# Kernel optimization log

Hardware: AMD Instinct MI355X
Metric: run time of the kernel (lower is better)

## Reference

```python
import jax, jax.numpy as jnp
import numpy as np

B, T, E, A = 16, 512, 256, 8

def setup_inputs() -> dict:
    key = jax.random.key(0)
    k1, k2, k3, k4, k5 = jax.random.split(key, 5)
    sent_feat = jax.random.normal(k1, (B, T, E), dtype=jnp.float32)
    mask = jax.random.randint(k2, (B, T), 0, 2, dtype=jnp.int32)
    atr_scores = jax.random.uniform(k3, (B, A), dtype=jnp.float32)
    W = jax.random.normal(k4, (E, A * E), dtype=jnp.float32) * 0.02  # nn.Linear weight (out, in)
    b = jax.random.normal(k5, (E,), dtype=jnp.float32) * 0.02
    return {"sent_feat": sent_feat, "mask": mask, "atr_scores": atr_scores, "W": W, "b": b}

def reference(sent_feat, mask, atr_scores, W, b):
    Bb, Tt, Ee = sent_feat.shape
    Aa = atr_scores.shape[1]
    sqrt_dim = jnp.float32(np.sqrt(Ee))
    # scale per-attribute copies of the sentence features: (B,A,T,E)
    sf = sent_feat[:, None, :, :] * atr_scores[:, :, None, None]
    sf = sf.reshape(Bb * Aa, Tt, Ee)
    # scaled dot-product scores (B*A, T, T)
    score = jnp.einsum('bte,bse->bts', sf, sf) / sqrt_dim
    # outer-product mask: bmm(mask[:,:,1], mask[:,1,:]) -> bool, repeat over A
    mf = mask.astype(jnp.float32)
    m2 = (mf[:, :, None] * mf[:, None, :]) != 0.0  # (B,T,T)
    m2 = jnp.broadcast_to(m2[:, None, :, :], (Bb, Aa, Tt, Tt)).reshape(Bb * Aa, Tt, Tt)
    # masked_fill_ fills score with 0.0 where mask == 0 (NOT -inf, faithful to source)
    score = jnp.where(m2, score, jnp.float32(0.0))
    # softmax(score - global_max) over last axis
    attn = jax.nn.softmax(score - jnp.max(score), axis=-1)
    attn_out = jnp.einsum('bts,bse->bte', attn, sf)  # (B*A, T, E)
    attn_out = attn_out.reshape(Bb, Tt, Aa * Ee)
    output = attn_out @ W.T + b  # (B, T, E)
    return (output, attn)
```

## Files before the change

kernel.cpp:

```cpp
#include <hip/hip_runtime.h>
#include <hip/hip_bf16.h>


#define Bt 16
#define Tt 512
#define Et 256
#define At 8

typedef __attribute__((ext_vector_type(8))) short short8;
typedef __attribute__((ext_vector_type(4))) float floatx4;

static __device__ __forceinline__ unsigned short f2bf(float x) {
    union { float f; unsigned u; } v; v.f = x;
    unsigned r = v.u + 0x7fffu + ((v.u >> 16) & 1u);
    return (unsigned short)(r >> 16);
}

static __device__ __forceinline__ floatx4 mfma16(short8 a, short8 b, floatx4 c) {
    return __builtin_amdgcn_mfma_f32_16x16x32_bf16(a, b, c, 0, 0, 0);
}

static __device__ __forceinline__ void barrier_lds() {
    __builtin_amdgcn_sched_barrier(0);
    asm volatile("s_waitcnt lgkmcnt(0)" ::: "memory");
    __builtin_amdgcn_s_barrier();
    __builtin_amdgcn_sched_barrier(0);
}

__global__ __launch_bounds__(256) void k_prep_sent(const float* __restrict__ sent,
                                                   unsigned short* __restrict__ sentG,
                                                   unsigned short* __restrict__ sentFB) {
    int bb = blockIdx.z;
    int s0 = blockIdx.x * 32;
    int e0 = blockIdx.y * 32;
    __shared__ float tile[32][33];
    int c  = threadIdx.x & 31;
    int r4 = threadIdx.x >> 5;
    for (int i = 0; i < 4; ++i) {
        int r = r4 + 8 * i;
        tile[r][c] = sent[(bb * Tt + s0 + r) * Et + e0 + c];
    }
    __syncthreads();
    int wv = threadIdx.x >> 6, lane = threadIdx.x & 63, quad = lane >> 4, l16 = lane & 15;
    union { short8 s; unsigned short e[8]; } u;
    if (wv < 2) {
#pragma unroll
        for (int j = 0; j < 8; ++j) u.e[j] = f2bf(tile[wv * 16 + l16][quad * 8 + j]);
        *(short8*)(sentG + (((size_t)(bb * 32 + (s0 >> 4) + wv)) * 8 + (e0 >> 5)) * 512
                   + lane * 8) = u.s;
    } else {
        int h = wv - 2;
#pragma unroll
        for (int j = 0; j < 8; ++j) u.e[j] = f2bf(tile[quad * 8 + j][h * 16 + l16]);
        *(short8*)(sentFB + (((size_t)(bb * 16 + (e0 >> 4) + h)) * 16 + (s0 >> 5)) * 512
                   + lane * 8) = u.s;
    }
}

__global__ __launch_bounds__(256) void k_prep_w(const float* __restrict__ W,
                                                unsigned short* __restrict__ Wp) {
    int nt = blockIdx.x;
    int pc = blockIdx.y;
    int wave = threadIdx.x >> 6, lane = threadIdx.x & 63, quad = lane >> 4, l16 = lane & 15;
    const int KK = At * Et;
    for (int p = pc * 2; p < pc * 2 + 2; ++p) {
        int kc = wave + 4 * p;
        const float* src = W + (size_t)(nt * 16 + l16) * KK + kc * 32 + quad * 8;
        union { short8 s; unsigned short e[8]; } u;
#pragma unroll
        for (int j = 0; j < 8; ++j) u.e[j] = f2bf(src[j]);
        *(short8*)(Wp + (((size_t)nt * 64 + kc) << 9) + lane * 8) = u.s;
    }
}

__global__ __launch_bounds__(256) void k_attnpv(const unsigned short* __restrict__ sentG,
                                                const unsigned short* __restrict__ sentFB,
                                                const int* __restrict__ mask,
                                                const float* __restrict__ atr,
                                                float* __restrict__ attnf,
                                                unsigned short* __restrict__ XwsF) {
    int hw = blockIdx.x;
    int logical = (hw & 7) * 128 + (hw >> 3);
    int bb = logical >> 6;
    int z  = (logical >> 5) & 1;
    int t0 = (logical & 31) * 16;
    int a0 = z * 4;
    __shared__ float S[16][516];
    __shared__ float msk[512];
    __shared__ float mrowv[16];
    unsigned short* Pb  = (unsigned short*)&S[0][0];
    unsigned short* Xb2 = Pb + 8192;

    int tid = threadIdx.x;
    for (int i = tid; i < 512; i += 256) msk[i] = (mask[bb * Tt + i] != 0) ? 1.0f : 0.0f;
    if (tid < 16) mrowv[tid] = (mask[bb * Tt + t0 + tid] != 0) ? 1.0f : 0.0f;
    barrier_lds();

    int wv = tid >> 6, lane = tid & 63, quad = lane >> 4, l16 = lane & 15;

    const unsigned short* Gbase = sentG + ((size_t)(bb * 32 + (t0 >> 4)) * 8) * 512 + lane * 8;
    short8 af[8];
#pragma unroll
    for (int kk = 0; kk < 8; ++kk) af[kk] = *(const short8*)(Gbase + kk * 512);

#pragma unroll
    for (int i = 0; i < 8; ++i) {
        int nt = wv * 8 + i;
        const unsigned short* Bb = sentG + ((size_t)(bb * 32 + nt) * 8) * 512 + lane * 8;
        floatx4 c = {0.f, 0.f, 0.f, 0.f};
#pragma unroll
        for (int kk = 0; kk < 8; ++kk)
            c = mfma16(af[kk], *(const short8*)(Bb + kk * 512), c);
#pragma unroll
        for (int r = 0; r < 4; ++r) {
            int cidx = nt * 16 + l16;
            S[quad * 4 + r][cidx] = c[r] * msk[cidx] * mrowv[quad * 4 + r];
        }
    }
    barrier_lds();

    int row = tid >> 4, cl = tid & 15;
    float w[32];
    float wmax = -1e30f;
#pragma unroll
    for (int i4 = 0; i4 < 8; ++i4) {
        float4 v = *(const float4*)&S[row][i4 * 64 + cl * 4];
        w[i4 * 4 + 0] = v.x; w[i4 * 4 + 1] = v.y; w[i4 * 4 + 2] = v.z; w[i4 * 4 + 3] = v.w;
        wmax = fmaxf(wmax, fmaxf(fmaxf(v.x, v.y), fmaxf(v.z, v.w)));
    }
#pragma unroll
    for (int off = 8; off >= 1; off >>= 1) wmax = fmaxf(wmax, __shfl_xor(wmax, off, 64));
    barrier_lds();

    int L = (t0 >> 3) & 15;

    for (int a = a0; a < a0 + 4; ++a) {
        float av = atr[bb * At + a];
        float coef = av * av * (1.0f / 16.0f);
        float mx = coef * wmax;
        float p[32];
        float sum = 0.f;
#pragma unroll
        for (int j = 0; j < 32; ++j) {
            float e = __expf(fmaf(coef, w[j], -mx));
            p[j] = e;
            sum += e;
        }
#pragma unroll
        for (int off = 8; off >= 1; off >>= 1) sum += __shfl_xor(sum, off, 64);
        float inv = 1.0f / sum;
#pragma unroll
        for (int j = 0; j < 32; ++j) p[j] *= inv;

        float* orow = attnf + ((size_t)(bb * At + a) * Tt + (t0 + row)) * Tt;
#pragma unroll
        for (int i4 = 0; i4 < 8; ++i4) {
            float4 v;
            v.x = p[i4 * 4 + 0]; v.y = p[i4 * 4 + 1];
            v.z = p[i4 * 4 + 2]; v.w = p[i4 * 4 + 3];
            *(float4*)(orow + i4 * 64 + cl * 4) = v;
        }

#pragma unroll
        for (int i4 = 0; i4 < 8; ++i4) {
            unsigned b0 = __float_as_uint(p[i4 * 4 + 0]) + 0x8000u;
            unsigned b1 = __float_as_uint(p[i4 * 4 + 1]) + 0x8000u;
            unsigned b2 = __float_as_uint(p[i4 * 4 + 2]) + 0x8000u;
            unsigned b3 = __float_as_uint(p[i4 * 4 + 3]) + 0x8000u;
            uint2 pk;
            pk.x = __builtin_amdgcn_perm(b1, b0, 0x07060302u);
            pk.y = __builtin_amdgcn_perm(b3, b2, 0x07060302u);
            int h = i4 * 8 + (cl >> 1);
            *(uint2*)(Pb + row * 512 + ((h ^ (row & 7)) << 3) + (cl & 1) * 4) = pk;
        }
        barrier_lds();

        floatx4 pacc[4];
#pragma unroll
        for (int i = 0; i < 4; ++i) pacc[i] = (floatx4){0.f, 0.f, 0.f, 0.f};
        for (int kc = 0; kc < 16; ++kc) {
            short8 afr = *(const short8*)(Pb + l16 * 512 +
                (((kc * 4 + quad) ^ (l16 & 7)) << 3));
#pragma unroll
            for (int i = 0; i < 4; ++i) {
                short8 bfr = *(const short8*)(sentFB +
                    (((size_t)(bb * 16 + wv * 4 + i) * 16 + kc) << 9) + lane * 8);
                pacc[i] = mfma16(afr, bfr, pacc[i]);
            }
        }

#pragma unroll
        for (int i = 0; i < 4; ++i) {
            int W16 = wv * 4 + i;
            int kcb = W16 >> 1;
            int qp  = (W16 & 1) * 2 + (l16 >> 3);
            int jp  = l16 & 7;
#pragma unroll
            for (int r = 0; r < 4; ++r) {
                int tl = quad * 4 + r;
                Xb2[(((tl & 7) * 8 + kcb) << 6) + qp * 16 + ((tl >> 3) << 3) + jp]
                    = f2bf(av * pacc[i][r]);
            }
        }
        barrier_lds();

        {
            int kc = tid >> 2, qp = tid & 3;
            int TPT = (a << 2) + (t0 >> 7);
            size_t base = (((size_t)(bb * 32 + TPT)) * 64 + kc) * 512;
            short8 v0 = *(const short8*)(Xb2 + (kc << 6) + qp * 16);
            short8 v1 = *(const short8*)(Xb2 + (kc << 6) + qp * 16 + 8);
            *(short8*)(XwsF + base + (qp * 16 + L) * 8)     = v0;
            *(short8*)(XwsF + base + (qp * 16 + L + 1) * 8) = v1;
        }
    }
}

__global__ __launch_bounds__(256) void k_out(const unsigned short* __restrict__ XwsF,
                                             const unsigned short* __restrict__ Wp,
                                             const float* __restrict__ bias,
                                             float* __restrict__ out) {
    int hw = blockIdx.x;
    int logical = (hw & 7) * 128 + (hw >> 3);
    int bb  = logical >> 6;
    int TPT = (logical >> 1) & 31;
    int nh  = logical & 1;
    int tid = threadIdx.x;
    int wv = tid >> 6, lane = tid & 63, quad = lane >> 4, l16 = lane & 15;

    const unsigned short* Abase = XwsF + ((size_t)(bb * 32 + TPT)) * 64 * 512 + lane * 8;
    floatx4 oacc[2];
    oacc[0] = (floatx4){0.f, 0.f, 0.f, 0.f};
    oacc[1] = (floatx4){0.f, 0.f, 0.f, 0.f};
    int nt0 = nh * 8 + wv * 2;
#pragma unroll 4
    for (int kc = 0; kc < 64; ++kc) {
        short8 afr = *(const short8*)(Abase + kc * 512);
#pragma unroll
        for (int i = 0; i < 2; ++i) {
            short8 bf = *(const short8*)(Wp +
                (((size_t)(nt0 + i) * 64 + kc) << 9) + lane * 8);
            oacc[i] = mfma16(afr, bf, oacc[i]);
        }
    }
#pragma unroll
    for (int i = 0; i < 2; ++i) {
        int n = (nt0 + i) * 16 + l16;
        float bv = bias[n];
#pragma unroll
        for (int r = 0; r < 4; ++r) {
            int tp = TPT * 16 + quad * 4 + r;
            out[((size_t)bb * Tt + tp) * Et + n] = oacc[i][r] + bv;
        }
    }
}

extern "C" void kernel_launch(void* const* d_in, const int* in_sizes, int n_in,
                              void* d_out, int out_size, void* d_ws, size_t ws_size,
                              hipStream_t stream) {
    const float* sent = (const float*)d_in[0];
    const int*   mask = (const int*)d_in[1];
    const float* atr  = (const float*)d_in[2];
    const float* W    = (const float*)d_in[3];
    const float* bias = (const float*)d_in[4];

    float* out0  = (float*)d_out;
    float* attnf = out0 + (size_t)Bt * Tt * Et;

    char* ws = (char*)d_ws;
    unsigned short* sentG  = (unsigned short*)(ws);
    unsigned short* sentFB = (unsigned short*)(ws + 4194304);
    unsigned short* Wp     = (unsigned short*)(ws + 8388608);
    unsigned short* XwsF   = (unsigned short*)(ws + 9437184);

    hipLaunchKernelGGL(k_prep_sent, dim3(Tt / 32, Et / 32, Bt), dim3(256), 0, stream,
                       sent, sentG, sentFB);
    hipLaunchKernelGGL(k_prep_w, dim3(16, 8), dim3(256), 0, stream, W, Wp);
    hipLaunchKernelGGL(k_attnpv, dim3(1024), dim3(256), 0, stream,
                       sentG, sentFB, mask, atr, attnf, XwsF);
    hipLaunchKernelGGL(k_out, dim3(1024), dim3(256), 0, stream,
                       XwsF, Wp, bias, out0);
}
```

Measured before the change: 232.6 us.

## Batch four attribute P tiles in LDS and share B-fragment loads across them

The attention-PV kernel now writes softmax probabilities for all four attributes into separate LDS tiles before a single barrier. It then runs one PV MFMA loop that loads each sentFB fragment once and reuses it across the four attributes, with a 4x4 accumulator array. Epilogue packing and global stores are also batched per attribute, which removes several barriers per attribute iteration. The cost is a larger LDS footprint (64 KB buffer) and 64 accumulator registers, which may reduce occupancy or cause spills.

```diff
diff --git a/kernel.cpp b/kernel.cpp
--- a/kernel.cpp
+++ b/kernel.cpp
@@ -85,11 +85,12 @@
     int z  = (logical >> 5) & 1;
     int t0 = (logical & 31) * 16;
     int a0 = z * 4;
-    __shared__ float S[16][516];
+
+    __shared__ __align__(16) float Sbuf[16384];
     __shared__ float msk[512];
     __shared__ float mrowv[16];
-    unsigned short* Pb  = (unsigned short*)&S[0][0];
-    unsigned short* Xb2 = Pb + 8192;
+    unsigned short* Pb  = (unsigned short*)Sbuf;
+    unsigned short* Xb2 = (unsigned short*)Sbuf;
 
     int tid = threadIdx.x;
     for (int i = tid; i < 512; i += 256) msk[i] = (mask[bb * Tt + i] != 0) ? 1.0f : 0.0f;
@@ -114,7 +115,7 @@
 #pragma unroll
         for (int r = 0; r < 4; ++r) {
             int cidx = nt * 16 + l16;
-            S[quad * 4 + r][cidx] = c[r] * msk[cidx] * mrowv[quad * 4 + r];
+            Sbuf[(quad * 4 + r) * 516 + cidx] = c[r] * msk[cidx] * mrowv[quad * 4 + r];
         }
     }
     barrier_lds();
@@ -124,7 +125,7 @@
     float wmax = -1e30f;
 #pragma unroll
     for (int i4 = 0; i4 < 8; ++i4) {
-        float4 v = *(const float4*)&S[row][i4 * 64 + cl * 4];
+        float4 v = *(const float4*)&Sbuf[row * 516 + i4 * 64 + cl * 4];
         w[i4 * 4 + 0] = v.x; w[i4 * 4 + 1] = v.y; w[i4 * 4 + 2] = v.z; w[i4 * 4 + 3] = v.w;
         wmax = fmaxf(wmax, fmaxf(fmaxf(v.x, v.y), fmaxf(v.z, v.w)));
     }
@@ -134,7 +135,9 @@
 
     int L = (t0 >> 3) & 15;
 
-    for (int a = a0; a < a0 + 4; ++a) {
+#pragma unroll
+    for (int al = 0; al < 4; ++al) {
+        int a = a0 + al;
         float av = atr[bb * At + a];
         float coef = av * av * (1.0f / 16.0f);
         float mx = coef * wmax;
@@ -171,24 +174,38 @@
             pk.x = __builtin_amdgcn_perm(b1, b0, 0x07060302u);
             pk.y = __builtin_amdgcn_perm(b3, b2, 0x07060302u);
             int h = i4 * 8 + (cl >> 1);
-            *(uint2*)(Pb + row * 512 + ((h ^ (row & 7)) << 3) + (cl & 1) * 4) = pk;
-        }
-        barrier_lds();
-
-        floatx4 pacc[4];
-#pragma unroll
-        for (int i = 0; i < 4; ++i) pacc[i] = (floatx4){0.f, 0.f, 0.f, 0.f};
-        for (int kc = 0; kc < 16; ++kc) {
-            short8 afr = *(const short8*)(Pb + l16 * 512 +
+            *(uint2*)(Pb + al * 8192 + row * 512 + ((h ^ (row & 7)) << 3)
+                      + (cl & 1) * 4) = pk;
+        }
+    }
+    barrier_lds();
+
+    floatx4 acc[4][4];
+#pragma unroll
+    for (int al = 0; al < 4; ++al)
+#pragma unroll
+        for (int i = 0; i < 4; ++i) acc[al][i] = (floatx4){0.f, 0.f, 0.f, 0.f};
+
+    for (int kc = 0; kc < 16; ++kc) {
+        short8 bfr[4];
+#pragma unroll
+        for (int i = 0; i < 4; ++i)
+            bfr[i] = *(const short8*)(sentFB +
+                (((size_t)(bb * 16 + wv * 4 + i) * 16 + kc) << 9) + lane * 8);
+#pragma unroll
+        for (int al = 0; al < 4; ++al) {
+            short8 afr = *(const short8*)(Pb + al * 8192 + l16 * 512 +
                 (((kc * 4 + quad) ^ (l16 & 7)) << 3));
 #pragma unroll
-            for (int i = 0; i < 4; ++i) {
-                short8 bfr = *(const short8*)(sentFB +
-                    (((size_t)(bb * 16 + wv * 4 + i) * 16 + kc) << 9) + lane * 8);
-                pacc[i] = mfma16(afr, bfr, pacc[i]);
-            }
-        }
-
+            for (int i = 0; i < 4; ++i)
+                acc[al][i] = mfma16(afr, bfr[i], acc[al][i]);
+        }
+    }
+    barrier_lds();
+
+#pragma unroll
+    for (int al = 0; al < 4; ++al) {
+        float av = atr[bb * At + a0 + al];
 #pragma unroll
         for (int i = 0; i < 4; ++i) {
             int W16 = wv * 4 + i;
@@ -198,21 +215,23 @@
 #pragma unroll
             for (int r = 0; r < 4; ++r) {
                 int tl = quad * 4 + r;
-                Xb2[(((tl & 7) * 8 + kcb) << 6) + qp * 16 + ((tl >> 3) << 3) + jp]
-                    = f2bf(av * pacc[i][r]);
+                Xb2[al * 4096 + (((tl & 7) * 8 + kcb) << 6) + qp * 16
+                    + ((tl >> 3) << 3) + jp] = f2bf(av * acc[al][i][r]);
             }
         }
-        barrier_lds();
-
-        {
-            int kc = tid >> 2, qp = tid & 3;
-            int TPT = (a << 2) + (t0 >> 7);
-            size_t base = (((size_t)(bb * 32 + TPT)) * 64 + kc) * 512;
-            short8 v0 = *(const short8*)(Xb2 + (kc << 6) + qp * 16);
-            short8 v1 = *(const short8*)(Xb2 + (kc << 6) + qp * 16 + 8);
-            *(short8*)(XwsF + base + (qp * 16 + L) * 8)     = v0;
-            *(short8*)(XwsF + base + (qp * 16 + L + 1) * 8) = v1;
-        }
+    }
+    barrier_lds();
+
+#pragma unroll
+    for (int al = 0; al < 4; ++al) {
+        int a = a0 + al;
+        int kc = tid >> 2, qp = tid & 3;
+        int TPT = (a << 2) + (t0 >> 7);
+        size_t base = (((size_t)(bb * 32 + TPT)) * 64 + kc) * 512;
+        short8 v0 = *(const short8*)(Xb2 + al * 4096 + (kc << 6) + qp * 16);
+        short8 v1 = *(const short8*)(Xb2 + al * 4096 + (kc << 6) + qp * 16 + 8);
+        *(short8*)(XwsF + base + (qp * 16 + L) * 8)     = v0;
+        *(short8*)(XwsF + base + (qp * 16 + L + 1) * 8) = v1;
     }
 }
 
```

New measurement: 219.1 us. 5.8% less time.
